# Optimization experiments

Measured on AMD Instinct MI355X. Metric: run time of the kernel, lower is better.

## Reference

```python
import jax, jax.numpy as jnp
import numpy as np

EPS = 1e-6
ROPE_THETA = 10000.0


def rmsnorm(x, w):
    return x * jax.lax.rsqrt(jnp.mean(x * x, axis=-1, keepdims=True) + EPS) * w


def rope(q, k, seq_len, head_dim):
    # rotate-half RoPE. q,k: [b, h, s, d]
    half = head_dim // 2
    inv_freq = 1.0 / (ROPE_THETA ** (jnp.arange(0, half, dtype=jnp.float32) / half))
    t = jnp.arange(seq_len, dtype=jnp.float32)
    freqs = jnp.outer(t, inv_freq)                      # [s, d/2]
    cos = jnp.concatenate([jnp.cos(freqs)] * 2, axis=-1)  # [s, d]
    sin = jnp.concatenate([jnp.sin(freqs)] * 2, axis=-1)

    def rot(x):
        x1, x2 = x[..., :half], x[..., half:]
        return jnp.concatenate([-x2, x1], axis=-1)

    return q * cos + rot(q) * sin, k * cos + rot(k) * sin


def setup_inputs() -> dict:
    key = jax.random.key(0)
    ks = jax.random.split(key, 8)
    B, S, D, E, F = 4, 2048, 1024, 8, 4096
    sd = 0.02
    return {
        "x": jax.random.normal(ks[0], (B, S, D), dtype=jnp.float32),
        "mapped_tokens": jax.random.randint(ks[1], (B, S), 0, E, dtype=jnp.int32),
        "rms1_w": jnp.ones((D,), dtype=jnp.float32),
        "wqkv": jax.random.normal(ks[2], (D, 3 * D), dtype=jnp.float32) * sd,
        "wo": jax.random.normal(ks[3], (D, D), dtype=jnp.float32) * sd,
        "rms2_w": jnp.ones((D,), dtype=jnp.float32),
        "w1": jax.random.normal(ks[4], (E, D, F), dtype=jnp.float32) * sd,
        "w2": jax.random.normal(ks[5], (E, F, D), dtype=jnp.float32) * sd,
    }


def attention(x, wqkv, wo, num_heads=16):
    B, S, D = x.shape
    hd = D // num_heads
    qkv = x @ wqkv                                       # [b, s, 3D]
    q, k, v = jnp.split(qkv, 3, axis=-1)
    def heads(t):
        return t.reshape(B, S, num_heads, hd).transpose(0, 2, 1, 3)  # [b,h,s,d]
    q, k, v = heads(q), heads(k), heads(v)
    q, k = rope(q, k, S, hd)
    scores = jnp.einsum("bhqd,bhkd->bhqk", q, k) / jnp.sqrt(jnp.float32(hd))
    causal = jnp.tril(jnp.ones((S, S), dtype=bool))
    scores = jnp.where(causal, scores, jnp.finfo(scores.dtype).min)
    attn = jax.nn.softmax(scores, axis=-1)
    out = jnp.einsum("bhqk,bhkd->bhqd", attn, v)
    out = out.transpose(0, 2, 1, 3).reshape(B, S, D)
    return out @ wo


def moe_hash_ffn(x, mapped_tokens, w1, w2):
    # hash-routed MoE: each token goes to exactly one expert given by mapped_tokens
    B, S, D = x.shape
    E = w1.shape[0]
    xf = x.reshape(B * S, D)
    mt = mapped_tokens.reshape(B * S)
    out = jnp.zeros_like(xf)
    for e in range(E):  # small fixed expert count
        y = jax.nn.gelu(xf @ w1[e]) @ w2[e]
        out = out + jnp.where((mt == e)[:, None], y, 0.0)
    return out.reshape(B, S, D)


def reference(x, mapped_tokens, rms1_w, wqkv, wo, rms2_w, w1, w2):
    h = x + attention(rmsnorm(x, rms1_w), wqkv, wo)
    out = h + moe_hash_ffn(rmsnorm(h, rms2_w), mapped_tokens, w1, w2)
    return out
```

## Files before the change

### kernel.cpp

```cpp
#include <hip/hip_runtime.h>
#include <hip/hip_bf16.h>
#include <stdint.h>

typedef __hip_bfloat16 bf16;
typedef __attribute__((ext_vector_type(8))) short bf16x8;
typedef __attribute__((ext_vector_type(4))) float f32x4;
typedef __attribute__((ext_vector_type(16))) float f32x16;
typedef unsigned int u32;

static constexpr int Bsz = 4, S = 2048, D = 1024, E = 8, F = 4096, NH = 16, HD = 64;
static constexpr int TOK = Bsz * S;
static constexpr int SLOTS = TOK + E * 128;

#define DEV __device__ __forceinline__

DEV void async16(const bf16* g, bf16* l) {
  __builtin_amdgcn_global_load_lds((const __attribute__((address_space(1))) u32*)g,
                                   (__attribute__((address_space(3))) u32*)l, 16, 0, 0);
}

DEV u32 lds_off(const bf16* p) {
  return (u32)(uintptr_t)(__attribute__((address_space(3))) bf16*)p;
}

DEV bf16x8 dsr128(u32 addr) {
  bf16x8 d;
  asm volatile("ds_read_b128 %0, %1" : "=v"(d) : "v"(addr));
  return d;
}

DEV float gelu_fast(float x) {
  const float z = 0.7978845608028654f * (x + 0.044715f * x * x * x);
  return x / (1.f + __expf(-2.f * z));
}

DEV u32 cvtpk(float lo, float hi) {
  u32 r;
  asm("v_cvt_pk_bf16_f32 %0, %1, %2" : "=v"(r) : "v"(lo), "v"(hi));
  return r;
}


__global__ void cvt_transpose(const float* __restrict__ in, bf16* __restrict__ out, int R, int C) {
  __shared__ float t[64][65];
  const size_t zoff = (size_t)blockIdx.z * R * C;
  const int c0 = blockIdx.x * 64, r0 = blockIdx.y * 64;
  const int tid = threadIdx.x;
  const int lrow = tid >> 4, lcol = (tid & 15) * 4;
#pragma unroll
  for (int p = 0; p < 4; ++p) {
    const int r = lrow + p * 16;
    const float4 v = *(const float4*)(in + zoff + (size_t)(r0 + r) * C + c0 + lcol);
    t[r][lcol] = v.x; t[r][lcol + 1] = v.y; t[r][lcol + 2] = v.z; t[r][lcol + 3] = v.w;
  }
  __syncthreads();
  const int ow = tid >> 3, je = (tid & 7) * 8;
#pragma unroll
  for (int p = 0; p < 2; ++p) {
    const int oc = ow + p * 32;
    union { bf16x8 v; bf16 b[8]; } o8;
#pragma unroll
    for (int j = 0; j < 8; ++j) o8.b[j] = __float2bfloat16(t[je + j][oc]);
    *(bf16x8*)(out + zoff + (size_t)(c0 + oc) * R + r0 + je) = o8.v;
  }
}

__global__ void rope_tables(float* __restrict__ cosT, float* __restrict__ sinT) {
  const int s = blockIdx.x * 2 + (threadIdx.x >> 5);
  const int i = threadIdx.x & 31;
  const float inv_freq = powf(10000.f, -(float)i / 32.f);
  const float ang = (float)s * inv_freq;
  cosT[s * 32 + i] = cosf(ang);
  sinT[s * 32 + i] = sinf(ang);
}

__global__ void rmsnorm_k(const float* __restrict__ x, const float* __restrict__ w, bf16* __restrict__ out) {
  const size_t row = blockIdx.x;
  const int tid = threadIdx.x;
  const float4 v = *(const float4*)(x + row * D + tid * 4);
  float ss = v.x * v.x + v.y * v.y + v.z * v.z + v.w * v.w;
#pragma unroll
  for (int off = 1; off < 64; off <<= 1) ss += __shfl_xor(ss, off);
  __shared__ float red[4];
  if ((tid & 63) == 0) red[tid >> 6] = ss;
  __syncthreads();
  const float inv = rsqrtf((red[0] + red[1] + red[2] + red[3]) * (1.f / D) + 1e-6f);
  const float4 wv = *(const float4*)(w + tid * 4);
  union { ushort4 u; bf16 b[4]; } o;
  o.b[0] = __float2bfloat16(v.x * inv * wv.x);
  o.b[1] = __float2bfloat16(v.y * inv * wv.y);
  o.b[2] = __float2bfloat16(v.z * inv * wv.z);
  o.b[3] = __float2bfloat16(v.w * inv * wv.w);
  *(ushort4*)((unsigned short*)out + row * D + tid * 4) = o.u;
}

__global__ void route_init(int* counts, int* cursors, int* perm) {
  const int i = blockIdx.x * 256 + threadIdx.x;
  if (i < E) { counts[i] = 0; cursors[i] = 0; }
  if (i < SLOTS) perm[i] = -1;
}
__global__ void route_count(const int* __restrict__ mt, int* counts) {
  const int i = blockIdx.x * 256 + threadIdx.x;
  if (i < TOK) atomicAdd(&counts[mt[i]], 1);
}
__global__ void route_offsets(const int* __restrict__ counts, int* aoff) {
  if (threadIdx.x == 0) {
    int off = 0; aoff[0] = 0;
    for (int e = 0; e < E; ++e) { off += (counts[e] + 127) & ~127; aoff[e + 1] = off; }
  }
}
__global__ void route_scatter(const int* __restrict__ mt, const int* __restrict__ aoff,
                              int* cursors, int* perm) {
  const int i = blockIdx.x * 256 + threadIdx.x;
  if (i < TOK) { const int e = mt[i]; perm[aoff[e] + atomicAdd(&cursors[e], 1)] = i; }
}

__global__ __launch_bounds__(512) void qkv8p(
    const bf16* __restrict__ A, const bf16* __restrict__ Bt,
    const float* __restrict__ c_t, const float* __restrict__ s_t,
    bf16* __restrict__ o_q, bf16* __restrict__ o_k, bf16* __restrict__ o_v) {
  constexpr int K = 1024, NT = K / 64;
  __shared__ __align__(16) bf16 LA[2][256 * 64];
  __shared__ __align__(16) bf16 LB[2][256 * 64];
  const int tid = threadIdx.x;
  const int lane = tid & 63, wv = tid >> 6;
  const int wm = wv >> 2, wn = wv & 3;
  const int rl = lane & 15, kg = lane >> 4;
  const int gx = gridDim.x;
  const int nwg = gx * gridDim.y;
  int bid = blockIdx.y * gx + blockIdx.x;
  bid = (bid & 7) * (nwg >> 3) + (bid >> 3);
  const int nbase = (bid % gx) * 256, mbase = (bid / gx) * 256;
  f32x4 acc[8][4] = {};
  const int srow = tid >> 3;
  const int sc = (tid & 7) ^ ((srow >> 1) & 7);
  const bf16* Ag = A + (size_t)(mbase + srow) * K + sc * 8;
  const bf16* Bg = Bt + (size_t)(nbase + srow) * K + sc * 8;

  auto stage = [&](int t, int h) {
    const int buf = t & 1;
    const int mat = h >> 1, rh = h & 1;
    const bf16* src = (mat ? Bg : Ag) + (size_t)(rh * 128) * K + t * 64;
    bf16* dst = (mat ? &LB[buf][0] : &LA[buf][0]) + rh * 128 * 64 + tid * 8;
    async16(src, dst);
    async16(src + (size_t)64 * K, dst + 64 * 64);
  };

  bf16x8 bfr[4];
  auto phaseC = [&](int t, int ks, int mih, bool loadB) {
    const int buf = t & 1;
    const u32 ab = lds_off(&LA[buf][0]);
    const u32 bb = lds_off(&LB[buf][0]);
    bf16x8 af[4];
#pragma unroll
    for (int mi = 0; mi < 4; ++mi) {
      const int row = wm * 128 + mih * 64 + mi * 16 + rl;
      const u32 ph = (u32)((ks * 4 + kg) ^ ((row >> 1) & 7));
      af[mi] = dsr128(ab + (u32)row * 128 + ph * 16);
    }
    if (loadB) {
#pragma unroll
      for (int ni = 0; ni < 4; ++ni) {
        const int row = wn * 64 + ni * 16 + rl;
        const u32 ph = (u32)((ks * 4 + kg) ^ ((row >> 1) & 7));
        bfr[ni] = dsr128(bb + (u32)row * 128 + ph * 16);
      }
    }
    asm volatile("s_waitcnt lgkmcnt(0)" ::: "memory");
    __builtin_amdgcn_sched_barrier(0);
    __builtin_amdgcn_s_setprio(1);
#pragma unroll
    for (int mi = 0; mi < 4; ++mi)
#pragma unroll
      for (int ni = 0; ni < 4; ++ni)
        acc[mih * 4 + mi][ni] =
            __builtin_amdgcn_mfma_f32_16x16x32_bf16(af[mi], bfr[ni], acc[mih * 4 + mi][ni], 0, 0, 0);
    __builtin_amdgcn_s_setprio(0);
  };

  stage(0, 0); stage(0, 1); stage(0, 2); stage(0, 3);
  for (int t = 0; t < NT; ++t) {
    const bool more = (t + 1 < NT);
#pragma unroll
    for (int p = 0; p < 4; ++p) {
      if (p == 0) {
        if (more) {
          stage(t + 1, 0);
          asm volatile("s_waitcnt vmcnt(2)" ::: "memory");
        } else {
          asm volatile("s_waitcnt vmcnt(0)" ::: "memory");
        }
        __builtin_amdgcn_s_barrier();
        __builtin_amdgcn_sched_barrier(0);
      } else if (more) {
        stage(t + 1, p);
      }
      phaseC(t, p >> 1, p & 1, (p & 1) == 0);
      __builtin_amdgcn_s_barrier();
      __builtin_amdgcn_sched_barrier(0);
    }
  }

  const int colbase = nbase + wn * 64;
  const int part = colbase >> 10;
  const int head = (colbase & 1023) >> 6;
  const float qs = (part == 0) ? 0.18033688011112042f : 1.f;
#pragma unroll
  for (int ai = 0; ai < 8; ++ai) {
    const int rowoff = (ai >> 2) * 64 + (ai & 3) * 16;
#pragma unroll
    for (int r = 0; r < 4; ++r) {
      const int grow = mbase + wm * 128 + rowoff + kg * 4 + r;
      const int bb = grow >> 11, sp = grow & (S - 1);
      if (part == 2) {
#pragma unroll
        for (int ni = 0; ni < 4; ++ni) {
          const int d = ni * 16 + rl;
          o_v[((size_t)(bb * NH + head) * HD + d) * S + sp] = __float2bfloat16(acc[ai][ni][r]);
        }
      } else {
        bf16* dst = (part == 0) ? o_q : o_k;
        const size_t base = ((size_t)(bb * NH + head) * S + sp) * HD;
#pragma unroll
        for (int np = 0; np < 2; ++np) {
          const int i = np * 16 + rl;
          const float c = c_t[sp * 32 + i];
          const float sn = s_t[sp * 32 + i];
          const float lo = acc[ai][np][r];
          const float hi = acc[ai][np + 2][r];
          dst[base + i] = __float2bfloat16((lo * c - hi * sn) * qs);
          dst[base + i + 32] = __float2bfloat16((hi * c + lo * sn) * qs);
        }
      }
    }
  }
}

template <int EPI, int BM>
__global__ __launch_bounds__(2 * BM) void gemm_bt(
    const bf16* __restrict__ A, const bf16* __restrict__ Bt, int M, int N, int K,
    const int* __restrict__ aoff, long long estride,
    const float* __restrict__ xres, float* __restrict__ o_h,
    bf16* __restrict__ o_act,
    const int* __restrict__ perm, const float* __restrict__ hres, float* __restrict__ o_out) {
  constexpr int WN = BM / 64;
  constexpr int MR = BM / 2;
  constexpr int M_FR = MR / 16;
  __shared__ __align__(16) bf16 As[2][BM * 32];
  __shared__ __align__(16) bf16 Bs[2][BM * 32];
  const int tid = threadIdx.x;
  const int lane = tid & 63, wv = tid >> 6;
  const int wm = wv / WN, wn = wv % WN;
  const int rl = lane & 15, kg = lane >> 4;
  const int gx = gridDim.x;
  const int nwg = gx * gridDim.y;
  int bid = blockIdx.y * gx + blockIdx.x;
  bid = (bid & 7) * (nwg >> 3) + (bid >> 3);
  const int nbase = (bid % gx) * BM, mbase = (bid / gx) * BM;
  const bf16* Btp = Bt;
  if constexpr (EPI >= 2) {
    int e = 0;
#pragma unroll
    for (int t = 0; t < E - 1; ++t) e += (mbase >= aoff[t + 1]) ? 1 : 0;
    Btp = Bt + (size_t)e * estride;
  }
  f32x4 acc[M_FR][4] = {};
  const int srow = tid >> 2;
  const int sc = (tid & 3) ^ ((srow >> 1) & 3);
  const bf16* Agp[2];
#pragma unroll
  for (int c = 0; c < 2; ++c) {
    int rowslot = mbase + c * MR + srow;
    if constexpr (EPI == 2) {
      const int t = perm[rowslot];
      rowslot = (t < 0) ? 0 : t;
    }
    Agp[c] = A + (size_t)rowslot * K + sc * 8;
  }
  const bf16* Bg = Btp + (size_t)(nbase + srow) * K + sc * 8;

  auto stage = [&](int bi, int ko) {
#pragma unroll
    for (int c = 0; c < 2; ++c) {
      async16(Agp[c] + ko, &As[bi][c * MR * 32 + wv * 512]);
      async16(Bg + (size_t)(c * MR) * K + ko, &Bs[bi][c * MR * 32 + wv * 512]);
    }
  };
  auto compute = [&](int bi) {
    bf16x8 af[M_FR], bfr[4];
#pragma unroll
    for (int mi = 0; mi < M_FR; ++mi) {
      const int row = wm * MR + mi * 16 + rl;
      af[mi] = *(const bf16x8*)&As[bi][row * 32 + ((kg ^ ((row >> 1) & 3))) * 8];
    }
#pragma unroll
    for (int ni = 0; ni < 4; ++ni) {
      const int row = wn * 64 + ni * 16 + rl;
      bfr[ni] = *(const bf16x8*)&Bs[bi][row * 32 + ((kg ^ ((row >> 1) & 3))) * 8];
    }
#pragma unroll
    for (int mi = 0; mi < M_FR; ++mi)
#pragma unroll
      for (int ni = 0; ni < 4; ++ni)
        acc[mi][ni] = __builtin_amdgcn_mfma_f32_16x16x32_bf16(af[mi], bfr[ni], acc[mi][ni], 0, 0, 0);
  };

  const int nk = K >> 5;
  stage(0, 0);
  __syncthreads();
  for (int kb = 0; kb < nk; ++kb) {
    if (kb + 1 < nk) stage((kb + 1) & 1, (kb + 1) * 32);
    compute(kb & 1);
    __syncthreads();
  }

#pragma unroll
  for (int mi = 0; mi < M_FR; ++mi) {
#pragma unroll
    for (int ni = 0; ni < 4; ++ni) {
#pragma unroll
      for (int r = 0; r < 4; ++r) {
        const int grow = mbase + wm * MR + mi * 16 + kg * 4 + r;
        const int gcol = nbase + wn * 64 + ni * 16 + rl;
        const float vv = acc[mi][ni][r];
        if constexpr (EPI == 1) {
          const size_t ix = (size_t)grow * 1024 + gcol;
          o_h[ix] = xres[ix] + vv;
        } else if constexpr (EPI == 2) {
          o_act[(size_t)grow * 4096 + gcol] = __float2bfloat16(gelu_fast(vv));
        } else {
          const int t = perm[grow];
          if (t >= 0) {
            const size_t ix = (size_t)t * 1024 + gcol;
            o_out[ix] = hres[ix] + vv;
          }
        }
      }
    }
  }
}

__global__ __launch_bounds__(128, 3) void attn_kernel(const bf16* __restrict__ Qb,
                                                      const bf16* __restrict__ Kb,
                                                      const bf16* __restrict__ Vt,
                                                      bf16* __restrict__ AO) {
  const int bh = blockIdx.x;
  const int w = threadIdx.x >> 6, lane = threadIdx.x & 63;
  const int q = lane & 31, hi = lane >> 5;
  const bf16* Qp = Qb + (size_t)bh * S * HD;
  const bf16* Kp = Kb + (size_t)bh * S * HD;
  const bf16* Vp = Vt + (size_t)bh * S * HD;
  const int b = bh >> 4, h = bh & 15;
  const int qt = (S / 32 - 1) - (blockIdx.y * 2 + w);
  const int qrow0 = qt * 32;
  bf16x8 qf[4];
#pragma unroll
  for (int t = 0; t < 4; ++t)
    qf[t] = *(const bf16x8*)(Qp + (size_t)(qrow0 + q) * HD + t * 16 + hi * 8);
  f32x16 oa0 = {}, oa1 = {};
  float m = -INFINITY, l = 0.f;
  const int nt = (qt + 2) >> 1;

  bf16x8 kf[8];
  auto loadK = [&](int kvb) {
#pragma unroll
    for (int t = 0; t < 4; ++t) {
      kf[t]     = *(const bf16x8*)(Kp + (size_t)(kvb + q) * HD + t * 16 + hi * 8);
      kf[4 + t] = *(const bf16x8*)(Kp + (size_t)(kvb + 32 + q) * HD + t * 16 + hi * 8);
    }
  };
  auto packP = [&](float s0, float s1, float s2, float s3,
                   float s4, float s5, float s6, float s7) -> bf16x8 {
    u32 x0 = cvtpk(s0, s1), x1 = cvtpk(s2, s3);
    u32 y0 = cvtpk(s4, s5), y1 = cvtpk(s6, s7);
    asm volatile("v_permlane32_swap_b32 %0, %1" : "+v"(x0), "+v"(y0));
    asm volatile("v_permlane32_swap_b32 %0, %1" : "+v"(x1), "+v"(y1));
    union { u32 w[4]; bf16x8 v; } u;
    u.w[0] = x0; u.w[1] = x1; u.w[2] = y0; u.w[3] = y1;
    return u.v;
  };

  loadK(0);
  for (int kt = 0; kt < nt; ++kt) {
    const int kvb = kt * 64;
    f32x16 sa0 = {}, sa1 = {};
#pragma unroll
    for (int t = 0; t < 4; ++t) sa0 = __builtin_amdgcn_mfma_f32_32x32x16_bf16(kf[t], qf[t], sa0, 0, 0, 0);
#pragma unroll
    for (int t = 0; t < 4; ++t) sa1 = __builtin_amdgcn_mfma_f32_32x32x16_bf16(kf[4 + t], qf[t], sa1, 0, 0, 0);
    bf16x8 vf0[4], vf1[4];
#pragma unroll
    for (int s2i = 0; s2i < 4; ++s2i) {
      vf0[s2i] = *(const bf16x8*)(Vp + (size_t)q * S + kvb + 16 * s2i + 8 * hi);
      vf1[s2i] = *(const bf16x8*)(Vp + (size_t)(32 + q) * S + kvb + 16 * s2i + 8 * hi);
    }
    if (kt + 1 < nt) loadK(kvb + 64);
    if (kvb + 63 > qrow0) {
#pragma unroll
      for (int r = 0; r < 16; ++r) {
        const int kloc = (r & 3) + 8 * (r >> 2) + 4 * hi;
        sa0[r] = (kvb + kloc > qrow0 + q) ? -3.0e38f : sa0[r];
        sa1[r] = (kvb + 32 + kloc > qrow0 + q) ? -3.0e38f : sa1[r];
      }
    }
    float vm;
    {
      float a0 = fmaxf(fmaxf(sa0[0], sa0[1]), fmaxf(sa0[2], sa0[3]));
      float a1 = fmaxf(fmaxf(sa0[4], sa0[5]), fmaxf(sa0[6], sa0[7]));
      float a2 = fmaxf(fmaxf(sa0[8], sa0[9]), fmaxf(sa0[10], sa0[11]));
      float a3 = fmaxf(fmaxf(sa0[12], sa0[13]), fmaxf(sa0[14], sa0[15]));
      float b0 = fmaxf(fmaxf(sa1[0], sa1[1]), fmaxf(sa1[2], sa1[3]));
      float b1 = fmaxf(fmaxf(sa1[4], sa1[5]), fmaxf(sa1[6], sa1[7]));
      float b2 = fmaxf(fmaxf(sa1[8], sa1[9]), fmaxf(sa1[10], sa1[11]));
      float b3 = fmaxf(fmaxf(sa1[12], sa1[13]), fmaxf(sa1[14], sa1[15]));
      vm = fmaxf(fmaxf(fmaxf(a0, a1), fmaxf(a2, a3)), fmaxf(fmaxf(b0, b1), fmaxf(b2, b3)));
    }
    vm = fmaxf(vm, __shfl_xor(vm, 32));
    const bool grow = __any(vm > m);
    const float mn = grow ? fmaxf(m, vm) : m;
#pragma unroll
    for (int r = 0; r < 16; ++r) {
      sa0[r] = exp2f(sa0[r] - mn);
      sa1[r] = exp2f(sa1[r] - mn);
    }
    float ps;
    {
      float a0 = (sa0[0] + sa0[1]) + (sa0[2] + sa0[3]);
      float a1 = (sa0[4] + sa0[5]) + (sa0[6] + sa0[7]);
      float a2 = (sa0[8] + sa0[9]) + (sa0[10] + sa0[11]);
      float a3 = (sa0[12] + sa0[13]) + (sa0[14] + sa0[15]);
      float b0 = (sa1[0] + sa1[1]) + (sa1[2] + sa1[3]);
      float b1 = (sa1[4] + sa1[5]) + (sa1[6] + sa1[7]);
      float b2 = (sa1[8] + sa1[9]) + (sa1[10] + sa1[11]);
      float b3 = (sa1[12] + sa1[13]) + (sa1[14] + sa1[15]);
      ps = ((a0 + a1) + (a2 + a3)) + ((b0 + b1) + (b2 + b3));
    }
    ps += __shfl_xor(ps, 32);
    if (grow) {
      const float scs = exp2f(m - mn);
      l = l * scs + ps;
      m = mn;
#pragma unroll
      for (int r = 0; r < 16; ++r) { oa0[r] *= scs; oa1[r] *= scs; }
    } else {
      l += ps;
    }
    {
      const bf16x8 pf0 = packP(sa0[0], sa0[1], sa0[2], sa0[3], sa0[4], sa0[5], sa0[6], sa0[7]);
      oa0 = __builtin_amdgcn_mfma_f32_32x32x16_bf16(vf0[0], pf0, oa0, 0, 0, 0);
      oa1 = __builtin_amdgcn_mfma_f32_32x32x16_bf16(vf1[0], pf0, oa1, 0, 0, 0);
      const bf16x8 pf1 = packP(sa0[8], sa0[9], sa0[10], sa0[11], sa0[12], sa0[13], sa0[14], sa0[15]);
      oa0 = __builtin_amdgcn_mfma_f32_32x32x16_bf16(vf0[1], pf1, oa0, 0, 0, 0);
      oa1 = __builtin_amdgcn_mfma_f32_32x32x16_bf16(vf1[1], pf1, oa1, 0, 0, 0);
      const bf16x8 pf2 = packP(sa1[0], sa1[1], sa1[2], sa1[3], sa1[4], sa1[5], sa1[6], sa1[7]);
      oa0 = __builtin_amdgcn_mfma_f32_32x32x16_bf16(vf0[2], pf2, oa0, 0, 0, 0);
      oa1 = __builtin_amdgcn_mfma_f32_32x32x16_bf16(vf1[2], pf2, oa1, 0, 0, 0);
      const bf16x8 pf3 = packP(sa1[8], sa1[9], sa1[10], sa1[11], sa1[12], sa1[13], sa1[14], sa1[15]);
      oa0 = __builtin_amdgcn_mfma_f32_32x32x16_bf16(vf0[3], pf3, oa0, 0, 0, 0);
      oa1 = __builtin_amdgcn_mfma_f32_32x32x16_bf16(vf1[3], pf3, oa1, 0, 0, 0);
    }
  }
  const float invl = 1.f / l;
#pragma unroll
  for (int n = 0; n < 2; ++n) {
#pragma unroll
    for (int g = 0; g < 4; ++g) {
      union { ushort4 u4; bf16 bb[4]; } o4;
#pragma unroll
      for (int mi = 0; mi < 4; ++mi) {
        const float val = (n ? oa1[4 * g + mi] : oa0[4 * g + mi]) * invl;
        o4.bb[mi] = __float2bfloat16(val);
      }
      const int d = n * 32 + 8 * g + 4 * hi;
      *(ushort4*)&AO[((size_t)(b * S + qrow0 + q)) * D + h * HD + d] = o4.u4;
    }
  }
}

extern "C" void kernel_launch(void* const* d_in, const int* in_sizes, int n_in,
                              void* d_out, int out_size, void* d_ws, size_t ws_size,
                              hipStream_t stream) {
  const float* x = (const float*)d_in[0];
  const int* mt = (const int*)d_in[1];
  const float* rms1 = (const float*)d_in[2];
  const float* wqkv = (const float*)d_in[3];
  const float* wo = (const float*)d_in[4];
  const float* rms2 = (const float*)d_in[5];
  const float* w1 = (const float*)d_in[6];
  const float* w2 = (const float*)d_in[7];
  float* out = (float*)d_out;
  (void)in_sizes; (void)n_in; (void)out_size; (void)ws_size;

  char* ws = (char*)d_ws;
  size_t off = 0;
  auto alloc = [&](size_t b) { void* p = ws + off; off = (off + b + 255) & ~(size_t)255; return p; };
  bf16* wqkvT = (bf16*)alloc((size_t)3072 * 1024 * 2);
  bf16* woT   = (bf16*)alloc((size_t)1024 * 1024 * 2);
  bf16* w1T   = (bf16*)alloc((size_t)E * F * D * 2);
  bf16* w2T   = (bf16*)alloc((size_t)E * D * F * 2);
  float* cosT = (float*)alloc((size_t)S * 32 * 4);
  float* sinT = (float*)alloc((size_t)S * 32 * 4);
  float* hbuf = (float*)alloc((size_t)TOK * D * 4);
  bf16* xn2   = (bf16*)alloc((size_t)TOK * D * 2);
  int* counts  = (int*)alloc(E * 4);
  int* cursors = (int*)alloc(E * 4);
  int* aoff    = (int*)alloc((E + 1) * 4);
  int* perm    = (int*)alloc(SLOTS * 4);
  char* R = (char*)alloc((size_t)5 * TOK * D * 2);
  bf16* xn = (bf16*)R;
  bf16* qb = (bf16*)(R + (size_t)1 * TOK * D * 2);
  bf16* kb = (bf16*)(R + (size_t)2 * TOK * D * 2);
  bf16* vb = (bf16*)(R + (size_t)3 * TOK * D * 2);
  bf16* ao = (bf16*)(R + (size_t)4 * TOK * D * 2);
  bf16* act = (bf16*)R;

  cvt_transpose<<<dim3(3072 / 64, 1024 / 64, 1), 256, 0, stream>>>(wqkv, wqkvT, 1024, 3072);
  cvt_transpose<<<dim3(1024 / 64, 1024 / 64, 1), 256, 0, stream>>>(wo, woT, 1024, 1024);
  cvt_transpose<<<dim3(4096 / 64, 1024 / 64, E), 256, 0, stream>>>(w1, w1T, 1024, 4096);
  cvt_transpose<<<dim3(1024 / 64, 4096 / 64, E), 256, 0, stream>>>(w2, w2T, 4096, 1024);
  rope_tables<<<dim3(S / 2), 64, 0, stream>>>(cosT, sinT);
  route_init<<<dim3((SLOTS + 255) / 256), 256, 0, stream>>>(counts, cursors, perm);
  route_count<<<dim3(TOK / 256), 256, 0, stream>>>(mt, counts);
  route_offsets<<<dim3(1), 64, 0, stream>>>(counts, aoff);
  route_scatter<<<dim3(TOK / 256), 256, 0, stream>>>(mt, aoff, cursors, perm);
  rmsnorm_k<<<dim3(TOK), 256, 0, stream>>>(x, rms1, xn);
  qkv8p<<<dim3(3072 / 256, TOK / 256), 512, 0, stream>>>(
      xn, wqkvT, cosT, sinT, qb, kb, vb);
  attn_kernel<<<dim3(64, S / 64), 128, 0, stream>>>(qb, kb, vb, ao);
  gemm_bt<1, 128><<<dim3(1024 / 128, TOK / 128), 256, 0, stream>>>(
      ao, woT, TOK, 1024, 1024, nullptr, 0, x, hbuf, nullptr, nullptr, nullptr, nullptr);
  rmsnorm_k<<<dim3(TOK), 256, 0, stream>>>(hbuf, rms2, xn2);
  gemm_bt<2, 128><<<dim3(4096 / 128, SLOTS / 128), 256, 0, stream>>>(
      xn2, w1T, SLOTS, 4096, 1024, aoff, (long long)F * D, nullptr, nullptr, act, perm,
      nullptr, nullptr);
  gemm_bt<3, 128><<<dim3(1024 / 128, SLOTS / 128), 256, 0, stream>>>(
      act, w2T, SLOTS, 1024, 4096, aoff, (long long)D * F, nullptr, nullptr, nullptr, perm,
      hbuf, out);
}
```

Baseline: 698.6 us.

## Share K/V tiles across four waves via double-buffered swizzled LDS in attention

The attention kernel now runs four waves per block covering 128 query rows. K and V tiles are staged cooperatively into double-buffered, XOR-swizzled LDS with async global-to-LDS loads, instead of each wave reading them straight from global memory. This cuts redundant global/L2 traffic for K/V and overlaps the next tile's load with compute. In exchange it adds a barrier every tile, and waves whose causal range has ended sit idle inside the block.

```diff
diff --git a/kernel.cpp b/kernel.cpp
--- a/kernel.cpp
+++ b/kernel.cpp
@@ -340,33 +340,41 @@
   }
 }
 
-__global__ __launch_bounds__(128, 3) void attn_kernel(const bf16* __restrict__ Qb,
+__global__ __launch_bounds__(256, 3) void attn_kernel(const bf16* __restrict__ Qb,
                                                       const bf16* __restrict__ Kb,
                                                       const bf16* __restrict__ Vt,
                                                       bf16* __restrict__ AO) {
+  __shared__ __align__(16) bf16 Kl[2][64 * 64];
+  __shared__ __align__(16) bf16 Vl[2][64 * 64];
   const int bh = blockIdx.x;
-  const int w = threadIdx.x >> 6, lane = threadIdx.x & 63;
+  const int tid = threadIdx.x;
+  const int w = tid >> 6, lane = tid & 63;
   const int q = lane & 31, hi = lane >> 5;
   const bf16* Qp = Qb + (size_t)bh * S * HD;
   const bf16* Kp = Kb + (size_t)bh * S * HD;
   const bf16* Vp = Vt + (size_t)bh * S * HD;
   const int b = bh >> 4, h = bh & 15;
-  const int qt = (S / 32 - 1) - (blockIdx.y * 2 + w);
-  const int qrow0 = qt * 32;
+  const int qblk = (S / 128 - 1) - blockIdx.y;
+  const int qrow0 = qblk * 128 + w * 32;
+  const int ntb = qblk * 2 + 2;
+  const int ntw = (qrow0 >> 6) + 1;
+  const int srow = tid >> 3;
+  const int schk = tid & 7;
+
   bf16x8 qf[4];
 #pragma unroll
   for (int t = 0; t < 4; ++t)
     qf[t] = *(const bf16x8*)(Qp + (size_t)(qrow0 + q) * HD + t * 16 + hi * 8);
   f32x16 oa0 = {}, oa1 = {};
   float m = -INFINITY, l = 0.f;
-  const int nt = (qt + 2) >> 1;
-
-  bf16x8 kf[8];
-  auto loadK = [&](int kvb) {
-#pragma unroll
-    for (int t = 0; t < 4; ++t) {
-      kf[t]     = *(const bf16x8*)(Kp + (size_t)(kvb + q) * HD + t * 16 + hi * 8);
-      kf[4 + t] = *(const bf16x8*)(Kp + (size_t)(kvb + 32 + q) * HD + t * 16 + hi * 8);
+
+  auto stageKV = [&](int buf, int kvb) {
+#pragma unroll
+    for (int hh = 0; hh < 2; ++hh) {
+      const int row = srow + hh * 32;
+      const int c = schk ^ (row & 7);
+      async16(Kp + (size_t)(kvb + row) * HD + c * 8, &Kl[buf][tid * 8 + hh * 2048]);
+      async16(Vp + (size_t)row * S + kvb + c * 8, &Vl[buf][tid * 8 + hh * 2048]);
     }
   };
   auto packP = [&](float s0, float s1, float s2, float s3,
@@ -380,85 +388,96 @@
     return u.v;
   };
 
-  loadK(0);
-  for (int kt = 0; kt < nt; ++kt) {
+  stageKV(0, 0);
+  __syncthreads();
+  for (int kt = 0; kt < ntb; ++kt) {
+    const int buf = kt & 1;
     const int kvb = kt * 64;
-    f32x16 sa0 = {}, sa1 = {};
-#pragma unroll
-    for (int t = 0; t < 4; ++t) sa0 = __builtin_amdgcn_mfma_f32_32x32x16_bf16(kf[t], qf[t], sa0, 0, 0, 0);
-#pragma unroll
-    for (int t = 0; t < 4; ++t) sa1 = __builtin_amdgcn_mfma_f32_32x32x16_bf16(kf[4 + t], qf[t], sa1, 0, 0, 0);
-    bf16x8 vf0[4], vf1[4];
-#pragma unroll
-    for (int s2i = 0; s2i < 4; ++s2i) {
-      vf0[s2i] = *(const bf16x8*)(Vp + (size_t)q * S + kvb + 16 * s2i + 8 * hi);
-      vf1[s2i] = *(const bf16x8*)(Vp + (size_t)(32 + q) * S + kvb + 16 * s2i + 8 * hi);
-    }
-    if (kt + 1 < nt) loadK(kvb + 64);
-    if (kvb + 63 > qrow0) {
+    if (kt + 1 < ntb) stageKV(buf ^ 1, kvb + 64);
+    if (kt < ntw) {
+      f32x16 sa0 = {}, sa1 = {};
+#pragma unroll
+      for (int t = 0; t < 4; ++t) {
+        const int c = (2 * t + hi) ^ (q & 7);
+        const bf16x8 kf0 = *(const bf16x8*)&Kl[buf][q * 64 + c * 8];
+        sa0 = __builtin_amdgcn_mfma_f32_32x32x16_bf16(kf0, qf[t], sa0, 0, 0, 0);
+      }
+#pragma unroll
+      for (int t = 0; t < 4; ++t) {
+        const int c = (2 * t + hi) ^ (q & 7);
+        const bf16x8 kf1 = *(const bf16x8*)&Kl[buf][(q + 32) * 64 + c * 8];
+        sa1 = __builtin_amdgcn_mfma_f32_32x32x16_bf16(kf1, qf[t], sa1, 0, 0, 0);
+      }
+      if (kvb + 63 > qrow0) {
+#pragma unroll
+        for (int r = 0; r < 16; ++r) {
+          const int kloc = (r & 3) + 8 * (r >> 2) + 4 * hi;
+          sa0[r] = (kvb + kloc > qrow0 + q) ? -3.0e38f : sa0[r];
+          sa1[r] = (kvb + 32 + kloc > qrow0 + q) ? -3.0e38f : sa1[r];
+        }
+      }
+      float vm;
+      {
+        float a0 = fmaxf(fmaxf(sa0[0], sa0[1]), fmaxf(sa0[2], sa0[3]));
+        float a1 = fmaxf(fmaxf(sa0[4], sa0[5]), fmaxf(sa0[6], sa0[7]));
+        float a2 = fmaxf(fmaxf(sa0[8], sa0[9]), fmaxf(sa0[10], sa0[11]));
+        float a3 = fmaxf(fmaxf(sa0[12], sa0[13]), fmaxf(sa0[14], sa0[15]));
+        float b0 = fmaxf(fmaxf(sa1[0], sa1[1]), fmaxf(sa1[2], sa1[3]));
+        float b1 = fmaxf(fmaxf(sa1[4], sa1[5]), fmaxf(sa1[6], sa1[7]));
+        float b2 = fmaxf(fmaxf(sa1[8], sa1[9]), fmaxf(sa1[10], sa1[11]));
+        float b3 = fmaxf(fmaxf(sa1[12], sa1[13]), fmaxf(sa1[14], sa1[15]));
+        vm = fmaxf(fmaxf(fmaxf(a0, a1), fmaxf(a2, a3)), fmaxf(fmaxf(b0, b1), fmaxf(b2, b3)));
+      }
+      vm = fmaxf(vm, __shfl_xor(vm, 32));
+      const bool grow = __any(vm > m);
+      const float mn = grow ? fmaxf(m, vm) : m;
 #pragma unroll
       for (int r = 0; r < 16; ++r) {
-        const int kloc = (r & 3) + 8 * (r >> 2) + 4 * hi;
-        sa0[r] = (kvb + kloc > qrow0 + q) ? -3.0e38f : sa0[r];
-        sa1[r] = (kvb + 32 + kloc > qrow0 + q) ? -3.0e38f : sa1[r];
-      }
-    }
-    float vm;
-    {
-      float a0 = fmaxf(fmaxf(sa0[0], sa0[1]), fmaxf(sa0[2], sa0[3]));
-      float a1 = fmaxf(fmaxf(sa0[4], sa0[5]), fmaxf(sa0[6], sa0[7]));
-      float a2 = fmaxf(fmaxf(sa0[8], sa0[9]), fmaxf(sa0[10], sa0[11]));
-      float a3 = fmaxf(fmaxf(sa0[12], sa0[13]), fmaxf(sa0[14], sa0[15]));
-      float b0 = fmaxf(fmaxf(sa1[0], sa1[1]), fmaxf(sa1[2], sa1[3]));
-      float b1 = fmaxf(fmaxf(sa1[4], sa1[5]), fmaxf(sa1[6], sa1[7]));
-      float b2 = fmaxf(fmaxf(sa1[8], sa1[9]), fmaxf(sa1[10], sa1[11]));
-      float b3 = fmaxf(fmaxf(sa1[12], sa1[13]), fmaxf(sa1[14], sa1[15]));
-      vm = fmaxf(fmaxf(fmaxf(a0, a1), fmaxf(a2, a3)), fmaxf(fmaxf(b0, b1), fmaxf(b2, b3)));
-    }
-    vm = fmaxf(vm, __shfl_xor(vm, 32));
-    const bool grow = __any(vm > m);
-    const float mn = grow ? fmaxf(m, vm) : m;
-#pragma unroll
-    for (int r = 0; r < 16; ++r) {
-      sa0[r] = exp2f(sa0[r] - mn);
-      sa1[r] = exp2f(sa1[r] - mn);
-    }
-    float ps;
-    {
-      float a0 = (sa0[0] + sa0[1]) + (sa0[2] + sa0[3]);
-      float a1 = (sa0[4] + sa0[5]) + (sa0[6] + sa0[7]);
-      float a2 = (sa0[8] + sa0[9]) + (sa0[10] + sa0[11]);
-      float a3 = (sa0[12] + sa0[13]) + (sa0[14] + sa0[15]);
-      float b0 = (sa1[0] + sa1[1]) + (sa1[2] + sa1[3]);
-      float b1 = (sa1[4] + sa1[5]) + (sa1[6] + sa1[7]);
-      float b2 = (sa1[8] + sa1[9]) + (sa1[10] + sa1[11]);
-      float b3 = (sa1[12] + sa1[13]) + (sa1[14] + sa1[15]);
-      ps = ((a0 + a1) + (a2 + a3)) + ((b0 + b1) + (b2 + b3));
-    }
-    ps += __shfl_xor(ps, 32);
-    if (grow) {
-      const float scs = exp2f(m - mn);
-      l = l * scs + ps;
-      m = mn;
-#pragma unroll
-      for (int r = 0; r < 16; ++r) { oa0[r] *= scs; oa1[r] *= scs; }
-    } else {
-      l += ps;
-    }
-    {
-      const bf16x8 pf0 = packP(sa0[0], sa0[1], sa0[2], sa0[3], sa0[4], sa0[5], sa0[6], sa0[7]);
-      oa0 = __builtin_amdgcn_mfma_f32_32x32x16_bf16(vf0[0], pf0, oa0, 0, 0, 0);
-      oa1 = __builtin_amdgcn_mfma_f32_32x32x16_bf16(vf1[0], pf0, oa1, 0, 0, 0);
-      const bf16x8 pf1 = packP(sa0[8], sa0[9], sa0[10], sa0[11], sa0[12], sa0[13], sa0[14], sa0[15]);
-      oa0 = __builtin_amdgcn_mfma_f32_32x32x16_bf16(vf0[1], pf1, oa0, 0, 0, 0);
-      oa1 = __builtin_amdgcn_mfma_f32_32x32x16_bf16(vf1[1], pf1, oa1, 0, 0, 0);
-      const bf16x8 pf2 = packP(sa1[0], sa1[1], sa1[2], sa1[3], sa1[4], sa1[5], sa1[6], sa1[7]);
-      oa0 = __builtin_amdgcn_mfma_f32_32x32x16_bf16(vf0[2], pf2, oa0, 0, 0, 0);
-      oa1 = __builtin_amdgcn_mfma_f32_32x32x16_bf16(vf1[2], pf2, oa1, 0, 0, 0);
-      const bf16x8 pf3 = packP(sa1[8], sa1[9], sa1[10], sa1[11], sa1[12], sa1[13], sa1[14], sa1[15]);
-      oa0 = __builtin_amdgcn_mfma_f32_32x32x16_bf16(vf0[3], pf3, oa0, 0, 0, 0);
-      oa1 = __builtin_amdgcn_mfma_f32_32x32x16_bf16(vf1[3], pf3, oa1, 0, 0, 0);
-    }
+        sa0[r] = exp2f(sa0[r] - mn);
+        sa1[r] = exp2f(sa1[r] - mn);
+      }
+      float ps;
+      {
+        float a0 = (sa0[0] + sa0[1]) + (sa0[2] + sa0[3]);
+        float a1 = (sa0[4] + sa0[5]) + (sa0[6] + sa0[7]);
+        float a2 = (sa0[8] + sa0[9]) + (sa0[10] + sa0[11]);
+        float a3 = (sa0[12] + sa0[13]) + (sa0[14] + sa0[15]);
+        float b0 = (sa1[0] + sa1[1]) + (sa1[2] + sa1[3]);
+        float b1 = (sa1[4] + sa1[5]) + (sa1[6] + sa1[7]);
+        float b2 = (sa1[8] + sa1[9]) + (sa1[10] + sa1[11]);
+        float b3 = (sa1[12] + sa1[13]) + (sa1[14] + sa1[15]);
+        ps = ((a0 + a1) + (a2 + a3)) + ((b0 + b1) + (b2 + b3));
+      }
+      ps += __shfl_xor(ps, 32);
+      if (grow) {
+        const float scs = exp2f(m - mn);
+        l = l * scs + ps;
+        m = mn;
+#pragma unroll
+        for (int r = 0; r < 16; ++r) { oa0[r] *= scs; oa1[r] *= scs; }
+      } else {
+        l += ps;
+      }
+      {
+        auto vrd = [&](int r, int s2i) -> bf16x8 {
+          const int c = (2 * s2i + hi) ^ (r & 7);
+          return *(const bf16x8*)&Vl[buf][r * 64 + c * 8];
+        };
+        const bf16x8 pf0 = packP(sa0[0], sa0[1], sa0[2], sa0[3], sa0[4], sa0[5], sa0[6], sa0[7]);
+        oa0 = __builtin_amdgcn_mfma_f32_32x32x16_bf16(vrd(q, 0), pf0, oa0, 0, 0, 0);
+        oa1 = __builtin_amdgcn_mfma_f32_32x32x16_bf16(vrd(q + 32, 0), pf0, oa1, 0, 0, 0);
+        const bf16x8 pf1 = packP(sa0[8], sa0[9], sa0[10], sa0[11], sa0[12], sa0[13], sa0[14], sa0[15]);
+        oa0 = __builtin_amdgcn_mfma_f32_32x32x16_bf16(vrd(q, 1), pf1, oa0, 0, 0, 0);
+        oa1 = __builtin_amdgcn_mfma_f32_32x32x16_bf16(vrd(q + 32, 1), pf1, oa1, 0, 0, 0);
+        const bf16x8 pf2 = packP(sa1[0], sa1[1], sa1[2], sa1[3], sa1[4], sa1[5], sa1[6], sa1[7]);
+        oa0 = __builtin_amdgcn_mfma_f32_32x32x16_bf16(vrd(q, 2), pf2, oa0, 0, 0, 0);
+        oa1 = __builtin_amdgcn_mfma_f32_32x32x16_bf16(vrd(q + 32, 2), pf2, oa1, 0, 0, 0);
+        const bf16x8 pf3 = packP(sa1[8], sa1[9], sa1[10], sa1[11], sa1[12], sa1[13], sa1[14], sa1[15]);
+        oa0 = __builtin_amdgcn_mfma_f32_32x32x16_bf16(vrd(q, 3), pf3, oa0, 0, 0, 0);
+        oa1 = __builtin_amdgcn_mfma_f32_32x32x16_bf16(vrd(q + 32, 3), pf3, oa1, 0, 0, 0);
+      }
+    }
+    __syncthreads();
   }
   const float invl = 1.f / l;
 #pragma unroll
@@ -526,7 +545,7 @@
   rmsnorm_k<<<dim3(TOK), 256, 0, stream>>>(x, rms1, xn);
   qkv8p<<<dim3(3072 / 256, TOK / 256), 512, 0, stream>>>(
       xn, wqkvT, cosT, sinT, qb, kb, vb);
-  attn_kernel<<<dim3(64, S / 64), 128, 0, stream>>>(qb, kb, vb, ao);
+  attn_kernel<<<dim3(64, S / 128), 256, 0, stream>>>(qb, kb, vb, ao);
   gemm_bt<1, 128><<<dim3(1024 / 128, TOK / 128), 256, 0, stream>>>(
       ao, woT, TOK, 1024, 1024, nullptr, 0, x, hbuf, nullptr, nullptr, nullptr, nullptr);
   rmsnorm_k<<<dim3(TOK), 256, 0, stream>>>(hbuf, rms2, xn2);
```

Measured after the change: 625.6 us. 10.5% less time.
